# Kernel optimization log

Hardware: AMD Instinct MI355X
Metric: run time of the kernel (lower is better)

## Reference

```python
import jax, jax.numpy as jnp
import numpy as np

EPS = 1e-5  # torch BatchNorm1d default eps
CATAGORY = 2


def setup_inputs() -> dict:
    key = jax.random.key(0)
    ks = jax.random.split(key, 8)
    B, N, D, P = 64, 512, 512, 720
    return {
        "x": jax.random.normal(ks[0], (B, N, D), dtype=jnp.float32),
        "W_exp": jax.random.normal(ks[1], (CATAGORY, D, P), dtype=jnp.float32) * 0.02,
        "b_exp": jax.random.normal(ks[2], (CATAGORY, P), dtype=jnp.float32) * 0.02,
        "W1": jax.random.normal(ks[3], (D, 128), dtype=jnp.float32) * 0.05,
        "b1": jnp.zeros((128,), jnp.float32),
        "g1": jnp.ones((128,), jnp.float32),
        "be1": jnp.zeros((128,), jnp.float32),
        "m1": jnp.zeros((128,), jnp.float32),
        "v1": jnp.ones((128,), jnp.float32),
        "W2": jax.random.normal(ks[4], (128, 32), dtype=jnp.float32) * 0.1,
        "b2": jnp.zeros((32,), jnp.float32),
        "g2": jnp.ones((32,), jnp.float32),
        "be2": jnp.zeros((32,), jnp.float32),
        "m2": jnp.zeros((32,), jnp.float32),
        "v2": jnp.ones((32,), jnp.float32),
        "W3": jax.random.normal(ks[5], (32, 1), dtype=jnp.float32) * 0.1,
        "b3": jnp.zeros((1,), jnp.float32),
    }


def _bn(h, gamma, beta, mean, var):
    # BatchNorm1d, eval mode (running stats); dropout is identity in eval
    return (h - mean) * jax.lax.rsqrt(var + EPS) * gamma + beta


def reference(x, W_exp, b_exp, W1, b1, g1, be1, m1, v1,
              W2, b2, g2, be2, m2, v2, W3, b3):
    B, N, D = x.shape
    xf = x.reshape(B * N, D)
    # classifier: Linear -> BN -> ReLU -> Linear -> BN -> ReLU -> Linear -> Sigmoid
    h = jax.nn.relu(_bn(xf @ W1 + b1, g1, be1, m1, v1))
    h = jax.nn.relu(_bn(h @ W2 + b2, g2, be2, m2, v2))
    z = jax.nn.sigmoid(h @ W3 + b3).reshape(B, N)  # [B, N] class score
    # per-token expert index (sigmoid score rounded to {0, 1})
    idx = jnp.clip(jnp.round(z), 0, CATAGORY - 1).astype(jnp.int32)  # [B, N]
    # compute all experts (catagory=2, cheap) then gather per-token choice
    outs = jnp.einsum("bnd,edp->bnep", x, W_exp) + b_exp  # [B, N, E, P]
    sel = jnp.take_along_axis(outs, idx[:, :, None, None], axis=2)
    return sel[:, :, 0, :]  # [B, N, pred_len]
```

## Files before the change

### kernel.cpp

```cpp
#include <hip/hip_runtime.h>

#define DEV __device__ __forceinline__

typedef __bf16 bf16x8 __attribute__((ext_vector_type(8)));
typedef float f32x4 __attribute__((ext_vector_type(4)));
typedef float f32x2 __attribute__((ext_vector_type(2)));

constexpr int TOK = 32768;
constexpr int D   = 512;
constexpr int P   = 720;
constexpr float EPS = 1e-5f;

DEV unsigned short f2bf(float f) {
  unsigned u = __float_as_uint(f);
  u += 0x7FFFu + ((u >> 16) & 1u);
  return (unsigned short)(u >> 16);
}

DEV void g2lds16(const void* g, void* l) {
  __builtin_amdgcn_global_load_lds(
      (__attribute__((address_space(1))) void*)g,
      (__attribute__((address_space(3))) void*)l, 16, 0, 0);
}

__global__ void wconv_kernel(const float* __restrict__ W,
                             unsigned short* __restrict__ WT) {
  __shared__ float ls[16][17];
  const int e  = blockIdx.z;
  const int d0 = blockIdx.x * 16, p0 = blockIdx.y * 16;
  const int tx = threadIdx.x, ty = threadIdx.y;
  ls[ty][tx] = W[((size_t)e * D + d0 + ty) * P + p0 + tx];
  __syncthreads();
  WT[((size_t)e * P + p0 + ty) * D + d0 + tx] = f2bf(ls[tx][ty]);
}

__global__ __launch_bounds__(256, 3) void classifier_kernel(
    const float* __restrict__ x,
    const float* __restrict__ W1, const float* __restrict__ b1,
    const float* __restrict__ g1, const float* __restrict__ be1,
    const float* __restrict__ m1, const float* __restrict__ v1,
    const float* __restrict__ W2, const float* __restrict__ b2,
    const float* __restrict__ g2, const float* __restrict__ be2,
    const float* __restrict__ m2, const float* __restrict__ v2,
    const float* __restrict__ W3, const float* __restrict__ b3,
    unsigned short* __restrict__ xb, unsigned long long* __restrict__ masks)
{
  constexpr int TM = 64, BK = 32;
  __shared__ __align__(16) char smem[50176];
  float (*xs)[32][68]  = (float(*)[32][68])smem;
  float (*ws)[32][128] = (float(*)[32][128])(smem + 17408);
  float (*h1s)[68]     = (float(*)[68])smem;
  float (*h2s)[68]     = (float(*)[68])(smem + 34816);

  const int tid  = threadIdx.x;
  const int wave = tid >> 6;
  const int lane = tid & 63;
  const int t0   = blockIdx.x * TM;

  const int xr = tid >> 2;
  const int xc = (tid & 3) * 4;
  const int tg = tid >> 4;
  const int cc = tid & 15;

  f32x2 acc[2][8];
  #pragma unroll
  for (int p = 0; p < 2; ++p)
    #pragma unroll
    for (int j = 0; j < 8; ++j) acc[p][j] = (f32x2)0.f;

  float4 px0, px1;

  auto issue_x = [&](int kt) {
    const float* base = &x[(size_t)(t0 + xr) * D + kt * BK + xc];
    px0 = *reinterpret_cast<const float4*>(base);
    px1 = *reinterpret_cast<const float4*>(base + 16);
  };
  auto commit_x = [&](int b, int kt) {
    xs[b][xc + 0][xr] = px0.x;  xs[b][xc + 1][xr] = px0.y;
    xs[b][xc + 2][xr] = px0.z;  xs[b][xc + 3][xr] = px0.w;
    xs[b][xc + 16][xr] = px1.x; xs[b][xc + 17][xr] = px1.y;
    xs[b][xc + 18][xr] = px1.z; xs[b][xc + 19][xr] = px1.w;
    ushort4 u0, u1;
    u0.x = f2bf(px0.x); u0.y = f2bf(px0.y); u0.z = f2bf(px0.z); u0.w = f2bf(px0.w);
    u1.x = f2bf(px1.x); u1.y = f2bf(px1.y); u1.z = f2bf(px1.z); u1.w = f2bf(px1.w);
    unsigned short* xbase = &xb[(size_t)(t0 + xr) * D + kt * BK + xc];
    *reinterpret_cast<ushort4*>(xbase)      = u0;
    *reinterpret_cast<ushort4*>(xbase + 16) = u1;
  };
  auto issue_w = [&](int b, int kt) {
    char* ldsbase = (char*)&ws[b][0][0];
    const int kk = (lane >> 5);
    const int ch = (lane & 31) * 4;
    #pragma unroll
    for (int i = 0; i < 4; ++i) {
      const int op = wave * 4 + i;
      g2lds16(&W1[(size_t)(kt * BK + op * 2 + kk) * 128 + ch],
              (char*)ldsbase + op * 1024);
    }
  };

  issue_w(0, 0);
  issue_x(0);
  commit_x(0, 0);
  __syncthreads();

  int buf = 0;
  for (int kt = 0; kt < D / BK; ++kt) {
    const int nb = buf ^ 1;
    if (kt < D / BK - 1) {
      issue_w(nb, kt + 1);
      issue_x(kt + 1);
    }
    #pragma unroll 4
    for (int kk = 0; kk < BK; ++kk) {
      const f32x4 xv = *reinterpret_cast<const f32x4*>(&xs[buf][kk][tg * 4]);
      const f32x4 wa = *reinterpret_cast<const f32x4*>(&ws[buf][kk][cc * 4]);
      const f32x4 wb = *reinterpret_cast<const f32x4*>(&ws[buf][kk][64 + cc * 4]);
      f32x2 xp[2];
      xp[0][0] = xv[0]; xp[0][1] = xv[1];
      xp[1][0] = xv[2]; xp[1][1] = xv[3];
      const float wr[8] = {wa[0], wa[1], wa[2], wa[3], wb[0], wb[1], wb[2], wb[3]};
      #pragma unroll
      for (int p = 0; p < 2; ++p)
        #pragma unroll
        for (int j = 0; j < 8; ++j) {
          f32x2 wv = {wr[j], wr[j]};
          acc[p][j] = __builtin_elementwise_fma(xp[p], wv, acc[p][j]);
        }
    }
    if (kt < D / BK - 1) commit_x(nb, kt + 1);
    __syncthreads();
    buf = nb;
  }

  #pragma unroll
  for (int j = 0; j < 8; ++j) {
    const int col = (j < 4) ? (cc * 4 + j) : (60 + cc * 4 + j);
    const float A  = g1[col] / sqrtf(v1[col] + EPS);
    const float Bc = (b1[col] - m1[col]) * A + be1[col];
    float4 hv;
    hv.x = fmaxf(0.f, fmaf(acc[0][j][0], A, Bc));
    hv.y = fmaxf(0.f, fmaf(acc[0][j][1], A, Bc));
    hv.z = fmaxf(0.f, fmaf(acc[1][j][0], A, Bc));
    hv.w = fmaxf(0.f, fmaf(acc[1][j][1], A, Bc));
    *reinterpret_cast<float4*>(&h1s[col][tg * 4]) = hv;
  }
  __syncthreads();

  {
    const int c2 = (tid & 7) * 4;
    const int t2 = (tid >> 3) * 2;
    f32x2 a2[4];
    #pragma unroll
    for (int c = 0; c < 4; ++c) a2[c] = (f32x2)0.f;
    #pragma unroll 8
    for (int j = 0; j < 128; ++j) {
      const f32x2 h = *reinterpret_cast<const f32x2*>(&h1s[j][t2]);
      const float4 w = *reinterpret_cast<const float4*>(&W2[j * 32 + c2]);
      const float wr[4] = {w.x, w.y, w.z, w.w};
      #pragma unroll
      for (int c = 0; c < 4; ++c) {
        f32x2 wv = {wr[c], wr[c]};
        a2[c] = __builtin_elementwise_fma(h, wv, a2[c]);
      }
    }
    #pragma unroll
    for (int c = 0; c < 4; ++c) {
      const int col = c2 + c;
      const float A  = g2[col] / sqrtf(v2[col] + EPS);
      const float Bc = (b2[col] - m2[col]) * A + be2[col];
      f32x2 hv;
      hv[0] = fmaxf(0.f, fmaf(a2[c][0], A, Bc));
      hv[1] = fmaxf(0.f, fmaf(a2[c][1], A, Bc));
      *reinterpret_cast<f32x2*>(&h2s[col][t2]) = hv;
    }
  }
  __syncthreads();

  if (tid < TM) {
    float logit = b3[0];
    #pragma unroll
    for (int k = 0; k < 32; ++k)
      logit = fmaf(h2s[k][tid], W3[k], logit);
    unsigned long long m = __ballot(logit > 0.f);
    if (tid == 0) masks[blockIdx.x] = m;
  }
}

__global__ __launch_bounds__(512) void scan_kernel(
    const unsigned long long* __restrict__ masks,
    int* __restrict__ off1s)
{
  __shared__ int s[512];
  const int t = threadIdx.x;
  const int c1 = __popcll(masks[t]);
  s[t] = c1;
  __syncthreads();
  #pragma unroll
  for (int d = 1; d < 512; d <<= 1) {
    int v = (t >= d) ? s[t - d] : 0;
    __syncthreads();
    s[t] += v;
    __syncthreads();
  }
  off1s[t] = s[t] - c1;
  if (t == 511) off1s[512] = s[511];
}

__global__ __launch_bounds__(256) void scatter_kernel(
    const unsigned long long* __restrict__ masks,
    const int* __restrict__ off1s,
    int* __restrict__ lists)
{
  const int wave = threadIdx.x >> 6;
  const int lane = threadIdx.x & 63;
  const int b = blockIdx.x * 4 + wave;
  const unsigned long long m = masks[b];
  const int off1 = off1s[b];
  const int off0 = b * 64 - off1;
  const int r1 = __popcll(m & ((1ull << lane) - 1ull));
  const int r0 = lane - r1;
  const int tok = b * 64 + lane;
  if ((m >> lane) & 1ull) lists[TOK + off1 + r1] = tok;
  else                    lists[off0 + r0] = tok;
}

__global__ __launch_bounds__(256) void expert_gemm_kernel(
    const unsigned short* __restrict__ xb,
    const unsigned short* __restrict__ WT,
    const float* __restrict__ b_exp,
    const int* __restrict__ off1s,
    const int* __restrict__ lists,
    float* __restrict__ out)
{
  constexpr int GM = 128, GN = 80, GK = 32;
  constexpr int NT = D / GK;
  __shared__ __align__(16) unsigned short As[4][GM * GK];
  __shared__ __align__(16) unsigned short Bs[4][GN * GK];

  const int tid  = threadIdx.x;
  const int wave = tid >> 6;
  const int lane = tid & 63;

  const int n1 = off1s[512];
  const int n0 = TOK - n1;
  const int T0 = (n0 + GM - 1) >> 7;
  const int T1 = (n1 + GM - 1) >> 7;

  const int wg    = blockIdx.x;
  const int xcd   = wg & 7;
  const int local = wg >> 3;
  const int gt    = xcd * 33 + local / 9;
  const int pt    = local % 9;
  if (gt >= T0 + T1) return;
  const int e  = (gt >= T0) ? 1 : 0;
  const int ne = e ? n1 : n0;
  const int m0 = (e ? gt - T0 : gt) * GM;
  const int p0 = pt * GN;
  const int* lst = lists + e * TOK;

  const int col  = lane & 15;
  const int rg   = lane >> 4;
  const int srow = lane >> 2;
  const int sswz = (lane & 3) ^ ((srow >> 1) & 3);

  int aid[2];
  #pragma unroll
  for (int i = 0; i < 2; ++i) {
    const int r = (wave + i * 4) * 16 + srow;
    int g = m0 + r; if (g > ne - 1) g = ne - 1;
    aid[i] = lst[g];
  }
  int eid[2][4]; unsigned evalid = 0;
  #pragma unroll
  for (int mf = 0; mf < 2; ++mf)
    #pragma unroll
    for (int j = 0; j < 4; ++j) {
      const int g = m0 + wave * 32 + mf * 16 + rg * 4 + j;
      const int gc = (g > ne - 1) ? ne - 1 : g;
      eid[mf][j] = lst[gc];
      if (g < ne) evalid |= 1u << (mf * 4 + j);
    }
  float be[5];
  #pragma unroll
  for (int nf = 0; nf < 5; ++nf)
    be[nf] = b_exp[e * P + p0 + nf * 16 + col];
  asm volatile("s_waitcnt vmcnt(0)" ::: "memory");

  f32x4 acc[2][5];
  #pragma unroll
  for (int mf = 0; mf < 2; ++mf)
    #pragma unroll
    for (int nf = 0; nf < 5; ++nf) acc[mf][nf] = (f32x4)(0.f);

  auto stage = [&](int b, int kt) {
    const int k0 = kt * GK;
    #pragma unroll
    for (int i = 0; i < 2; ++i) {
      const int c = wave + i * 4;
      g2lds16(xb + (size_t)aid[i] * D + k0 + sswz * 8,
              (char*)As[b] + c * 1024);
    }
    {
      const int pr = wave * 16 + srow;
      g2lds16(WT + ((size_t)e * P + p0 + pr) * D + k0 + sswz * 8,
              (char*)Bs[b] + wave * 1024);
    }
    if (wave == 0) {
      const int pr = 64 + srow;
      g2lds16(WT + ((size_t)e * P + p0 + pr) * D + k0 + sswz * 8,
              (char*)Bs[b] + 4 * 1024);
    }
  };

  stage(0, 0);
  stage(1, 1);
  stage(2, 2);

  #pragma unroll
  for (int kt = 0; kt < NT; ++kt) {
    if (kt < NT - 2) {
      if (wave == 0) asm volatile("s_waitcnt vmcnt(8)" ::: "memory");
      else           asm volatile("s_waitcnt vmcnt(6)" ::: "memory");
    } else if (kt == NT - 2) {
      if (wave == 0) asm volatile("s_waitcnt vmcnt(4)" ::: "memory");
      else           asm volatile("s_waitcnt vmcnt(3)" ::: "memory");
    } else {
      asm volatile("s_waitcnt vmcnt(0)" ::: "memory");
    }
    __builtin_amdgcn_s_barrier();
    __builtin_amdgcn_sched_barrier(0);

    if (kt + 3 < NT) stage((kt + 3) & 3, kt + 3);

    const int buf = kt & 3;
    bf16x8 af[2];
    #pragma unroll
    for (int mf = 0; mf < 2; ++mf) {
      const int r  = wave * 32 + mf * 16 + (lane & 15);
      const int ch = (lane >> 4) ^ ((r >> 1) & 3);
      af[mf] = *(const bf16x8*)((const char*)As[buf] + r * 64 + ch * 16);
    }
    #pragma unroll
    for (int nf = 0; nf < 5; ++nf) {
      const int pr = nf * 16 + (lane & 15);
      const int ch = (lane >> 4) ^ ((pr >> 1) & 3);
      bf16x8 bfrag = *(const bf16x8*)((const char*)Bs[buf] + pr * 64 + ch * 16);
      #pragma unroll
      for (int mf = 0; mf < 2; ++mf)
        acc[mf][nf] = __builtin_amdgcn_mfma_f32_16x16x32_bf16(
            af[mf], bfrag, acc[mf][nf], 0, 0, 0);
    }
  }

  #pragma unroll
  for (int nf = 0; nf < 5; ++nf) {
    const int p = p0 + nf * 16 + col;
    #pragma unroll
    for (int mf = 0; mf < 2; ++mf) {
      #pragma unroll
      for (int j = 0; j < 4; ++j) {
        if (evalid & (1u << (mf * 4 + j)))
          out[(size_t)eid[mf][j] * P + p] = acc[mf][nf][j] + be[nf];
      }
    }
  }
}

extern "C" void kernel_launch(void* const* d_in, const int* in_sizes, int n_in,
                              void* d_out, int out_size, void* d_ws, size_t ws_size,
                              hipStream_t stream) {
  const float* x     = (const float*)d_in[0];
  const float* W_exp = (const float*)d_in[1];
  const float* b_exp = (const float*)d_in[2];
  const float* W1 = (const float*)d_in[3];
  const float* b1 = (const float*)d_in[4];
  const float* g1 = (const float*)d_in[5];
  const float* be1 = (const float*)d_in[6];
  const float* m1 = (const float*)d_in[7];
  const float* v1 = (const float*)d_in[8];
  const float* W2 = (const float*)d_in[9];
  const float* b2 = (const float*)d_in[10];
  const float* g2 = (const float*)d_in[11];
  const float* be2 = (const float*)d_in[12];
  const float* m2 = (const float*)d_in[13];
  const float* v2 = (const float*)d_in[14];
  const float* W3 = (const float*)d_in[15];
  const float* b3 = (const float*)d_in[16];
  float* out = (float*)d_out;

  char* wsb = (char*)d_ws;
  unsigned short* xb = (unsigned short*)wsb;
  unsigned short* WT = (unsigned short*)(wsb + 33554432);
  unsigned long long* masks = (unsigned long long*)(wsb + 35028992);
  int* off1s = (int*)(wsb + 35033088);
  int* lists = (int*)(wsb + 35036160);

  hipLaunchKernelGGL(wconv_kernel, dim3(D / 16, P / 16, 2), dim3(16, 16),
                     0, stream, W_exp, WT);
  hipLaunchKernelGGL(classifier_kernel, dim3(TOK / 64), dim3(256), 0, stream,
                     x, W1, b1, g1, be1, m1, v1, W2, b2, g2, be2, m2, v2, W3, b3,
                     xb, masks);
  hipLaunchKernelGGL(scan_kernel, dim3(1), dim3(512), 0, stream, masks, off1s);
  hipLaunchKernelGGL(scatter_kernel, dim3(128), dim3(256), 0, stream,
                     masks, off1s, lists);
  hipLaunchKernelGGL(expert_gemm_kernel, dim3(8 * 33 * 9), dim3(256),
                     0, stream, xb, WT, b_exp, off1s, lists, out);
}
```

Baseline: 131.8 us.

## Use 4x16 register tile with split-K across half-blocks in classifier GEMM

Reorganizes the classifier's first-layer GEMM so each thread computes a 4x16 output tile instead of 4x8, with the two halves of the block each handling half of every K slice. The partial sums are then reduced through shared memory before BN/ReLU. This raises arithmetic intensity per LDS load and cuts redundant weight and x reads. It costs more registers, which is why launch bounds drop to 2 blocks per SM, plus an extra sync and an LDS round trip for the reduction.

Measured after the change: 134.0 us. Within noise of the previous version (+1.7%).

```diff
diff --git a/kernel.cpp b/kernel.cpp
--- a/kernel.cpp
+++ b/kernel.cpp
@@ -34,7 +34,7 @@
   WT[((size_t)e * P + p0 + ty) * D + d0 + tx] = f2bf(ls[tx][ty]);
 }
 
-__global__ __launch_bounds__(256, 3) void classifier_kernel(
+__global__ __launch_bounds__(256, 2) void classifier_kernel(
     const float* __restrict__ x,
     const float* __restrict__ W1, const float* __restrict__ b1,
     const float* __restrict__ g1, const float* __restrict__ be1,
@@ -59,14 +59,17 @@
 
   const int xr = tid >> 2;
   const int xc = (tid & 3) * 4;
-  const int tg = tid >> 4;
-  const int cc = tid & 15;
-
-  f32x2 acc[2][8];
-  #pragma unroll
-  for (int p = 0; p < 2; ++p)
-    #pragma unroll
-    for (int j = 0; j < 8; ++j) acc[p][j] = (f32x2)0.f;
+
+  const int kb = (tid >> 7) * 16;
+  const int th = tid & 127;
+  const int tg = th >> 3;
+  const int cg = th & 7;
+
+  float acc[4][16];
+  #pragma unroll
+  for (int i = 0; i < 4; ++i)
+    #pragma unroll
+    for (int j = 0; j < 16; ++j) acc[i][j] = 0.f;
 
   float4 px0, px1;
 
@@ -111,39 +114,51 @@
       issue_w(nb, kt + 1);
       issue_x(kt + 1);
     }
-    #pragma unroll 4
-    for (int kk = 0; kk < BK; ++kk) {
-      const f32x4 xv = *reinterpret_cast<const f32x4*>(&xs[buf][kk][tg * 4]);
-      const f32x4 wa = *reinterpret_cast<const f32x4*>(&ws[buf][kk][cc * 4]);
-      const f32x4 wb = *reinterpret_cast<const f32x4*>(&ws[buf][kk][64 + cc * 4]);
-      f32x2 xp[2];
-      xp[0][0] = xv[0]; xp[0][1] = xv[1];
-      xp[1][0] = xv[2]; xp[1][1] = xv[3];
-      const float wr[8] = {wa[0], wa[1], wa[2], wa[3], wb[0], wb[1], wb[2], wb[3]};
+    #pragma unroll 2
+    for (int kk = 0; kk < 16; ++kk) {
+      const f32x4 xv = *reinterpret_cast<const f32x4*>(&xs[buf][kb + kk][tg * 4]);
+      const f32x4 w0 = *reinterpret_cast<const f32x4*>(&ws[buf][kb + kk][cg * 16 + 0]);
+      const f32x4 w1 = *reinterpret_cast<const f32x4*>(&ws[buf][kb + kk][cg * 16 + 4]);
+      const f32x4 w2 = *reinterpret_cast<const f32x4*>(&ws[buf][kb + kk][cg * 16 + 8]);
+      const f32x4 w3 = *reinterpret_cast<const f32x4*>(&ws[buf][kb + kk][cg * 16 + 12]);
+      const float xr4[4] = {xv[0], xv[1], xv[2], xv[3]};
+      const float wr[16] = {w0[0], w0[1], w0[2], w0[3],
+                            w1[0], w1[1], w1[2], w1[3],
+                            w2[0], w2[1], w2[2], w2[3],
+                            w3[0], w3[1], w3[2], w3[3]};
       #pragma unroll
-      for (int p = 0; p < 2; ++p)
+      for (int i = 0; i < 4; ++i)
         #pragma unroll
-        for (int j = 0; j < 8; ++j) {
-          f32x2 wv = {wr[j], wr[j]};
-          acc[p][j] = __builtin_elementwise_fma(xp[p], wv, acc[p][j]);
-        }
+        for (int j = 0; j < 16; ++j)
+          acc[i][j] = fmaf(xr4[i], wr[j], acc[i][j]);
     }
     if (kt < D / BK - 1) commit_x(nb, kt + 1);
     __syncthreads();
     buf = nb;
   }
 
-  #pragma unroll
-  for (int j = 0; j < 8; ++j) {
-    const int col = (j < 4) ? (cc * 4 + j) : (60 + cc * 4 + j);
-    const float A  = g1[col] / sqrtf(v1[col] + EPS);
-    const float Bc = (b1[col] - m1[col]) * A + be1[col];
-    float4 hv;
-    hv.x = fmaxf(0.f, fmaf(acc[0][j][0], A, Bc));
-    hv.y = fmaxf(0.f, fmaf(acc[0][j][1], A, Bc));
-    hv.z = fmaxf(0.f, fmaf(acc[1][j][0], A, Bc));
-    hv.w = fmaxf(0.f, fmaf(acc[1][j][1], A, Bc));
-    *reinterpret_cast<float4*>(&h1s[col][tg * 4]) = hv;
+  if (kb) {
+    #pragma unroll
+    for (int j = 0; j < 16; ++j) {
+      float4 v = {acc[0][j], acc[1][j], acc[2][j], acc[3][j]};
+      *reinterpret_cast<float4*>(&h1s[cg * 16 + j][tg * 4]) = v;
+    }
+  }
+  __syncthreads();
+  if (!kb) {
+    #pragma unroll
+    for (int j = 0; j < 16; ++j) {
+      const int col = cg * 16 + j;
+      const float4 hp = *reinterpret_cast<const float4*>(&h1s[col][tg * 4]);
+      const float A  = g1[col] / sqrtf(v1[col] + EPS);
+      const float Bc = (b1[col] - m1[col]) * A + be1[col];
+      float4 hv;
+      hv.x = fmaxf(0.f, fmaf(acc[0][j] + hp.x, A, Bc));
+      hv.y = fmaxf(0.f, fmaf(acc[1][j] + hp.y, A, Bc));
+      hv.z = fmaxf(0.f, fmaf(acc[2][j] + hp.z, A, Bc));
+      hv.w = fmaxf(0.f, fmaf(acc[3][j] + hp.w, A, Bc));
+      *reinterpret_cast<float4*>(&h1s[col][tg * 4]) = hv;
+    }
   }
   __syncthreads();
 
```

## Enlarge classifier token tile to 128 with 8x8 register microtile

Applied to the files above, without the earlier changes.

The classifier's first-layer GEMM now uses 128-token tiles with BK=16, and each thread accumulates an 8x8 register microtile instead of 4x8. This raises arithmetic intensity per LDS read and halves the grid, and the W1 tile is reused across twice as many tokens. The second and third layers then run in two 64-token halves that reuse the existing 64-wide scratch buffers. The cost is more registers per thread, since launch bounds drop the 3-block occupancy hint, plus extra syncs in the epilogue.

After: 144.2 us. 9.4% more time.

```diff
diff --git a/kernel.cpp b/kernel.cpp
--- a/kernel.cpp
+++ b/kernel.cpp
@@ -34,7 +34,7 @@
   WT[((size_t)e * P + p0 + ty) * D + d0 + tx] = f2bf(ls[tx][ty]);
 }
 
-__global__ __launch_bounds__(256, 3) void classifier_kernel(
+__global__ __launch_bounds__(256) void classifier_kernel(
     const float* __restrict__ x,
     const float* __restrict__ W1, const float* __restrict__ b1,
     const float* __restrict__ g1, const float* __restrict__ be1,
@@ -45,10 +45,10 @@
     const float* __restrict__ W3, const float* __restrict__ b3,
     unsigned short* __restrict__ xb, unsigned long long* __restrict__ masks)
 {
-  constexpr int TM = 64, BK = 32;
-  __shared__ __align__(16) char smem[50176];
-  float (*xs)[32][68]  = (float(*)[32][68])smem;
-  float (*ws)[32][128] = (float(*)[32][128])(smem + 17408);
+  constexpr int TM = 128, BK = 16, NTILE = D / BK;
+  __shared__ __align__(16) char smem[43520];
+  float (*xs)[16][132] = (float(*)[16][132])smem;
+  float (*ws)[16][128] = (float(*)[16][128])(smem + 16896);
   float (*h1s)[68]     = (float(*)[68])smem;
   float (*h2s)[68]     = (float(*)[68])(smem + 34816);
 
@@ -57,43 +57,44 @@
   const int lane = tid & 63;
   const int t0   = blockIdx.x * TM;
 
-  const int xr = tid >> 2;
-  const int xc = (tid & 3) * 4;
+  const int xr = tid >> 1;
+  const int xc = (tid & 1) * 8;
+
   const int tg = tid >> 4;
   const int cc = tid & 15;
 
-  f32x2 acc[2][8];
-  #pragma unroll
-  for (int p = 0; p < 2; ++p)
-    #pragma unroll
-    for (int j = 0; j < 8; ++j) acc[p][j] = (f32x2)0.f;
+  float acc[8][8];
+  #pragma unroll
+  for (int i = 0; i < 8; ++i)
+    #pragma unroll
+    for (int j = 0; j < 8; ++j) acc[i][j] = 0.f;
 
   float4 px0, px1;
 
   auto issue_x = [&](int kt) {
     const float* base = &x[(size_t)(t0 + xr) * D + kt * BK + xc];
     px0 = *reinterpret_cast<const float4*>(base);
-    px1 = *reinterpret_cast<const float4*>(base + 16);
+    px1 = *reinterpret_cast<const float4*>(base + 4);
   };
   auto commit_x = [&](int b, int kt) {
-    xs[b][xc + 0][xr] = px0.x;  xs[b][xc + 1][xr] = px0.y;
-    xs[b][xc + 2][xr] = px0.z;  xs[b][xc + 3][xr] = px0.w;
-    xs[b][xc + 16][xr] = px1.x; xs[b][xc + 17][xr] = px1.y;
-    xs[b][xc + 18][xr] = px1.z; xs[b][xc + 19][xr] = px1.w;
+    xs[b][xc + 0][xr] = px0.x; xs[b][xc + 1][xr] = px0.y;
+    xs[b][xc + 2][xr] = px0.z; xs[b][xc + 3][xr] = px0.w;
+    xs[b][xc + 4][xr] = px1.x; xs[b][xc + 5][xr] = px1.y;
+    xs[b][xc + 6][xr] = px1.z; xs[b][xc + 7][xr] = px1.w;
     ushort4 u0, u1;
     u0.x = f2bf(px0.x); u0.y = f2bf(px0.y); u0.z = f2bf(px0.z); u0.w = f2bf(px0.w);
     u1.x = f2bf(px1.x); u1.y = f2bf(px1.y); u1.z = f2bf(px1.z); u1.w = f2bf(px1.w);
     unsigned short* xbase = &xb[(size_t)(t0 + xr) * D + kt * BK + xc];
-    *reinterpret_cast<ushort4*>(xbase)      = u0;
-    *reinterpret_cast<ushort4*>(xbase + 16) = u1;
+    *reinterpret_cast<ushort4*>(xbase)     = u0;
+    *reinterpret_cast<ushort4*>(xbase + 4) = u1;
   };
   auto issue_w = [&](int b, int kt) {
     char* ldsbase = (char*)&ws[b][0][0];
     const int kk = (lane >> 5);
     const int ch = (lane & 31) * 4;
     #pragma unroll
-    for (int i = 0; i < 4; ++i) {
-      const int op = wave * 4 + i;
+    for (int i = 0; i < 2; ++i) {
+      const int op = wave * 2 + i;
       g2lds16(&W1[(size_t)(kt * BK + op * 2 + kk) * 128 + ch],
               (char*)ldsbase + op * 1024);
     }
@@ -105,85 +106,94 @@
   __syncthreads();
 
   int buf = 0;
-  for (int kt = 0; kt < D / BK; ++kt) {
+  for (int kt = 0; kt < NTILE; ++kt) {
     const int nb = buf ^ 1;
-    if (kt < D / BK - 1) {
+    if (kt < NTILE - 1) {
       issue_w(nb, kt + 1);
       issue_x(kt + 1);
     }
-    #pragma unroll 4
+    #pragma unroll 8
     for (int kk = 0; kk < BK; ++kk) {
-      const f32x4 xv = *reinterpret_cast<const f32x4*>(&xs[buf][kk][tg * 4]);
+      const f32x4 xa = *reinterpret_cast<const f32x4*>(&xs[buf][kk][tg * 8]);
+      const f32x4 xbv = *reinterpret_cast<const f32x4*>(&xs[buf][kk][tg * 8 + 4]);
       const f32x4 wa = *reinterpret_cast<const f32x4*>(&ws[buf][kk][cc * 4]);
       const f32x4 wb = *reinterpret_cast<const f32x4*>(&ws[buf][kk][64 + cc * 4]);
-      f32x2 xp[2];
-      xp[0][0] = xv[0]; xp[0][1] = xv[1];
-      xp[1][0] = xv[2]; xp[1][1] = xv[3];
-      const float wr[8] = {wa[0], wa[1], wa[2], wa[3], wb[0], wb[1], wb[2], wb[3]};
-      #pragma unroll
-      for (int p = 0; p < 2; ++p)
+      const float xr8[8] = {xa[0], xa[1], xa[2], xa[3], xbv[0], xbv[1], xbv[2], xbv[3]};
+      const float wr8[8] = {wa[0], wa[1], wa[2], wa[3], wb[0], wb[1], wb[2], wb[3]};
+      #pragma unroll
+      for (int i = 0; i < 8; ++i)
         #pragma unroll
-        for (int j = 0; j < 8; ++j) {
-          f32x2 wv = {wr[j], wr[j]};
-          acc[p][j] = __builtin_elementwise_fma(xp[p], wv, acc[p][j]);
+        for (int j = 0; j < 8; ++j)
+          acc[i][j] = fmaf(xr8[i], wr8[j], acc[i][j]);
+    }
+    if (kt < NTILE - 1) commit_x(nb, kt + 1);
+    __syncthreads();
+    buf = nb;
+  }
+
+  #pragma unroll 1
+  for (int h = 0; h < 2; ++h) {
+    if ((tg >> 3) == h) {
+      const int tl = (tg & 7) * 8;
+      #pragma unroll
+      for (int j = 0; j < 8; ++j) {
+        const int col = (j < 4) ? (cc * 4 + j) : (60 + cc * 4 + j);
+        const float A  = g1[col] / sqrtf(v1[col] + EPS);
+        const float Bc = (b1[col] - m1[col]) * A + be1[col];
+        float4 h0, h1v;
+        h0.x = fmaxf(0.f, fmaf(acc[0][j], A, Bc));
+        h0.y = fmaxf(0.f, fmaf(acc[1][j], A, Bc));
+        h0.z = fmaxf(0.f, fmaf(acc[2][j], A, Bc));
+        h0.w = fmaxf(0.f, fmaf(acc[3][j], A, Bc));
+        h1v.x = fmaxf(0.f, fmaf(acc[4][j], A, Bc));
+        h1v.y = fmaxf(0.f, fmaf(acc[5][j], A, Bc));
+        h1v.z = fmaxf(0.f, fmaf(acc[6][j], A, Bc));
+        h1v.w = fmaxf(0.f, fmaf(acc[7][j], A, Bc));
+        *reinterpret_cast<float4*>(&h1s[col][tl])     = h0;
+        *reinterpret_cast<float4*>(&h1s[col][tl + 4]) = h1v;
+      }
+    }
+    __syncthreads();
+
+    {
+      const int c2 = (tid & 7) * 4;
+      const int t2 = (tid >> 3) * 2;
+      f32x2 a2[4];
+      #pragma unroll
+      for (int c = 0; c < 4; ++c) a2[c] = (f32x2)0.f;
+      #pragma unroll 8
+      for (int j = 0; j < 128; ++j) {
+        const f32x2 hv = *reinterpret_cast<const f32x2*>(&h1s[j][t2]);
+        const float4 w = *reinterpret_cast<const float4*>(&W2[j * 32 + c2]);
+        const float wr[4] = {w.x, w.y, w.z, w.w};
+        #pragma unroll
+        for (int c = 0; c < 4; ++c) {
+          f32x2 wv = {wr[c], wr[c]};
+          a2[c] = __builtin_elementwise_fma(hv, wv, a2[c]);
         }
-    }
-    if (kt < D / BK - 1) commit_x(nb, kt + 1);
-    __syncthreads();
-    buf = nb;
-  }
-
-  #pragma unroll
-  for (int j = 0; j < 8; ++j) {
-    const int col = (j < 4) ? (cc * 4 + j) : (60 + cc * 4 + j);
-    const float A  = g1[col] / sqrtf(v1[col] + EPS);
-    const float Bc = (b1[col] - m1[col]) * A + be1[col];
-    float4 hv;
-    hv.x = fmaxf(0.f, fmaf(acc[0][j][0], A, Bc));
-    hv.y = fmaxf(0.f, fmaf(acc[0][j][1], A, Bc));
-    hv.z = fmaxf(0.f, fmaf(acc[1][j][0], A, Bc));
-    hv.w = fmaxf(0.f, fmaf(acc[1][j][1], A, Bc));
-    *reinterpret_cast<float4*>(&h1s[col][tg * 4]) = hv;
-  }
-  __syncthreads();
-
-  {
-    const int c2 = (tid & 7) * 4;
-    const int t2 = (tid >> 3) * 2;
-    f32x2 a2[4];
-    #pragma unroll
-    for (int c = 0; c < 4; ++c) a2[c] = (f32x2)0.f;
-    #pragma unroll 8
-    for (int j = 0; j < 128; ++j) {
-      const f32x2 h = *reinterpret_cast<const f32x2*>(&h1s[j][t2]);
-      const float4 w = *reinterpret_cast<const float4*>(&W2[j * 32 + c2]);
-      const float wr[4] = {w.x, w.y, w.z, w.w};
+      }
       #pragma unroll
       for (int c = 0; c < 4; ++c) {
-        f32x2 wv = {wr[c], wr[c]};
-        a2[c] = __builtin_elementwise_fma(h, wv, a2[c]);
+        const int col = c2 + c;
+        const float A  = g2[col] / sqrtf(v2[col] + EPS);
+        const float Bc = (b2[col] - m2[col]) * A + be2[col];
+        f32x2 hv;
+        hv[0] = fmaxf(0.f, fmaf(a2[c][0], A, Bc));
+        hv[1] = fmaxf(0.f, fmaf(a2[c][1], A, Bc));
+        *reinterpret_cast<f32x2*>(&h2s[col][t2]) = hv;
       }
     }
-    #pragma unroll
-    for (int c = 0; c < 4; ++c) {
-      const int col = c2 + c;
-      const float A  = g2[col] / sqrtf(v2[col] + EPS);
-      const float Bc = (b2[col] - m2[col]) * A + be2[col];
-      f32x2 hv;
-      hv[0] = fmaxf(0.f, fmaf(a2[c][0], A, Bc));
-      hv[1] = fmaxf(0.f, fmaf(a2[c][1], A, Bc));
-      *reinterpret_cast<f32x2*>(&h2s[col][t2]) = hv;
-    }
-  }
-  __syncthreads();
-
-  if (tid < TM) {
-    float logit = b3[0];
-    #pragma unroll
-    for (int k = 0; k < 32; ++k)
-      logit = fmaf(h2s[k][tid], W3[k], logit);
-    unsigned long long m = __ballot(logit > 0.f);
-    if (tid == 0) masks[blockIdx.x] = m;
+    __syncthreads();
+
+    if (tid < 64) {
+      float logit = b3[0];
+      #pragma unroll
+      for (int k = 0; k < 32; ++k)
+        logit = fmaf(h2s[k][tid], W3[k], logit);
+      unsigned long long m = __ballot(logit > 0.f);
+      if (tid == 0) masks[blockIdx.x * 2 + h] = m;
+    }
+    __syncthreads();
   }
 }
 
@@ -398,7 +408,7 @@
 
   hipLaunchKernelGGL(wconv_kernel, dim3(D / 16, P / 16, 2), dim3(16, 16),
                      0, stream, W_exp, WT);
-  hipLaunchKernelGGL(classifier_kernel, dim3(TOK / 64), dim3(256), 0, stream,
+  hipLaunchKernelGGL(classifier_kernel, dim3(TOK / 128), dim3(256), 0, stream,
                      x, W1, b1, g1, be1, m1, v1, W2, b2, g2, be2, m2, v2, W3, b3,
                      xb, masks);
   hipLaunchKernelGGL(scan_kernel, dim3(1), dim3(512), 0, stream, masks, off1s);
```

## Use 8x8 register tiles with split-K across thread halves in classifier GEMM

Applied to the files above, without the earlier changes.

The first classifier layer's FMA loop changes from a 4x8 per-thread tile over all 32 k-values to an 8x8 tile over half the k-slice. The two 128-thread halves each handle 16 k-values and then combine their partial sums through shared memory before BN/ReLU. This raises the FMA count per LDS load, lowering shared-memory traffic relative to compute. In exchange it adds an extra reduction step with a barrier and more accumulator registers, which may reduce occupancy.

Result: faster. 127.6 us (-3.2%).

```diff
diff --git a/kernel.cpp b/kernel.cpp
--- a/kernel.cpp
+++ b/kernel.cpp
@@ -59,14 +59,17 @@
 
   const int xr = tid >> 2;
   const int xc = (tid & 3) * 4;
-  const int tg = tid >> 4;
-  const int cc = tid & 15;
-
-  f32x2 acc[2][8];
-  #pragma unroll
-  for (int p = 0; p < 2; ++p)
-    #pragma unroll
-    for (int j = 0; j < 8; ++j) acc[p][j] = (f32x2)0.f;
+
+  const int kb = (tid >> 7) * 16;
+  const int th = tid & 127;
+  const int tg = th >> 4;
+  const int cg = th & 15;
+
+  float acc[8][8];
+  #pragma unroll
+  for (int i = 0; i < 8; ++i)
+    #pragma unroll
+    for (int j = 0; j < 8; ++j) acc[i][j] = 0.f;
 
   float4 px0, px1;
 
@@ -112,38 +115,58 @@
       issue_x(kt + 1);
     }
     #pragma unroll 4
-    for (int kk = 0; kk < BK; ++kk) {
-      const f32x4 xv = *reinterpret_cast<const f32x4*>(&xs[buf][kk][tg * 4]);
-      const f32x4 wa = *reinterpret_cast<const f32x4*>(&ws[buf][kk][cc * 4]);
-      const f32x4 wb = *reinterpret_cast<const f32x4*>(&ws[buf][kk][64 + cc * 4]);
-      f32x2 xp[2];
-      xp[0][0] = xv[0]; xp[0][1] = xv[1];
-      xp[1][0] = xv[2]; xp[1][1] = xv[3];
-      const float wr[8] = {wa[0], wa[1], wa[2], wa[3], wb[0], wb[1], wb[2], wb[3]};
+    for (int kk = 0; kk < 16; ++kk) {
+      const int kr = kb + kk;
+      const f32x4 xa  = *reinterpret_cast<const f32x4*>(&xs[buf][kr][tg * 8]);
+      const f32x4 xv2 = *reinterpret_cast<const f32x4*>(&xs[buf][kr][tg * 8 + 4]);
+      const f32x4 wa  = *reinterpret_cast<const f32x4*>(&ws[buf][kr][cg * 4]);
+      const f32x4 wb  = *reinterpret_cast<const f32x4*>(&ws[buf][kr][64 + cg * 4]);
+      const float xr8[8] = {xa[0], xa[1], xa[2], xa[3],
+                            xv2[0], xv2[1], xv2[2], xv2[3]};
+      const float wr8[8] = {wa[0], wa[1], wa[2], wa[3],
+                            wb[0], wb[1], wb[2], wb[3]};
       #pragma unroll
-      for (int p = 0; p < 2; ++p)
+      for (int i = 0; i < 8; ++i)
         #pragma unroll
-        for (int j = 0; j < 8; ++j) {
-          f32x2 wv = {wr[j], wr[j]};
-          acc[p][j] = __builtin_elementwise_fma(xp[p], wv, acc[p][j]);
-        }
+        for (int j = 0; j < 8; ++j)
+          acc[i][j] = fmaf(xr8[i], wr8[j], acc[i][j]);
     }
     if (kt < D / BK - 1) commit_x(nb, kt + 1);
     __syncthreads();
     buf = nb;
   }
 
-  #pragma unroll
-  for (int j = 0; j < 8; ++j) {
-    const int col = (j < 4) ? (cc * 4 + j) : (60 + cc * 4 + j);
-    const float A  = g1[col] / sqrtf(v1[col] + EPS);
-    const float Bc = (b1[col] - m1[col]) * A + be1[col];
-    float4 hv;
-    hv.x = fmaxf(0.f, fmaf(acc[0][j][0], A, Bc));
-    hv.y = fmaxf(0.f, fmaf(acc[0][j][1], A, Bc));
-    hv.z = fmaxf(0.f, fmaf(acc[1][j][0], A, Bc));
-    hv.w = fmaxf(0.f, fmaf(acc[1][j][1], A, Bc));
-    *reinterpret_cast<float4*>(&h1s[col][tg * 4]) = hv;
+  if (kb) {
+    #pragma unroll
+    for (int j = 0; j < 8; ++j) {
+      const int col = (j < 4) ? (cg * 4 + j) : (60 + cg * 4 + j);
+      float4 p0 = {acc[0][j], acc[1][j], acc[2][j], acc[3][j]};
+      float4 p1 = {acc[4][j], acc[5][j], acc[6][j], acc[7][j]};
+      *reinterpret_cast<float4*>(&h1s[col][tg * 8])     = p0;
+      *reinterpret_cast<float4*>(&h1s[col][tg * 8 + 4]) = p1;
+    }
+  }
+  __syncthreads();
+  if (!kb) {
+    #pragma unroll
+    for (int j = 0; j < 8; ++j) {
+      const int col = (j < 4) ? (cg * 4 + j) : (60 + cg * 4 + j);
+      const float4 q0 = *reinterpret_cast<const float4*>(&h1s[col][tg * 8]);
+      const float4 q1 = *reinterpret_cast<const float4*>(&h1s[col][tg * 8 + 4]);
+      const float A  = g1[col] / sqrtf(v1[col] + EPS);
+      const float Bc = (b1[col] - m1[col]) * A + be1[col];
+      float4 h0, h1v;
+      h0.x = fmaxf(0.f, fmaf(acc[0][j] + q0.x, A, Bc));
+      h0.y = fmaxf(0.f, fmaf(acc[1][j] + q0.y, A, Bc));
+      h0.z = fmaxf(0.f, fmaf(acc[2][j] + q0.z, A, Bc));
+      h0.w = fmaxf(0.f, fmaf(acc[3][j] + q0.w, A, Bc));
+      h1v.x = fmaxf(0.f, fmaf(acc[4][j] + q1.x, A, Bc));
+      h1v.y = fmaxf(0.f, fmaf(acc[5][j] + q1.y, A, Bc));
+      h1v.z = fmaxf(0.f, fmaf(acc[6][j] + q1.z, A, Bc));
+      h1v.w = fmaxf(0.f, fmaf(acc[7][j] + q1.w, A, Bc));
+      *reinterpret_cast<float4*>(&h1s[col][tg * 8])     = h0;
+      *reinterpret_cast<float4*>(&h1s[col][tg * 8 + 4]) = h1v;
+    }
   }
   __syncthreads();
 
```
